# Performance work log

Hardware: AMD Instinct MI355X
Metric: run time of the kernel (lower is better)

## Reference

```python
import jax, jax.numpy as jnp
import numpy as np

KSIZE = 8
STRIDE = 4
HEADS = 8
DIM_HEAD = 32
EPS = 1e-5


def _layernorm(x, g, b):
    m = jnp.mean(x, axis=-1, keepdims=True)
    v = jnp.mean(jnp.square(x - m), axis=-1, keepdims=True)
    return (x - m) / jnp.sqrt(v + EPS) * g + b


def setup_inputs() -> dict:
    key = jax.random.key(0)
    ks = jax.random.split(key, 4)
    B, H, W, C = 8, 64, 64, 256
    inner = HEADS * DIM_HEAD  # 256
    x = jax.random.normal(ks[0], (B, H, W, C), dtype=jnp.float32)
    return {
        "x": x,
        "ln1_g": jnp.ones((C,), jnp.float32),
        "ln1_b": jnp.zeros((C,), jnp.float32),
        "ln2_g": jnp.ones((C,), jnp.float32),
        "ln2_b": jnp.zeros((C,), jnp.float32),
        "w_qkv": jax.random.normal(ks[1], (C, inner * 3), jnp.float32) * 0.02,
        "w_out": jax.random.normal(ks[2], (inner, C), jnp.float32) * 0.02,
        "b_out": jnp.zeros((C,), jnp.float32),
    }


def reference(x, ln1_g, ln1_b, ln2_g, ln2_b, w_qkv, w_out, b_out):
    B, H, W, C = x.shape
    k, s = KSIZE, STRIDE
    nH = (H - k) // s + 1
    nW = (W - k) // s + 1
    L = nH * nW
    n = k * k  # tokens per window

    # window index grids (im2col / unfold)
    rows = jnp.arange(nH)[:, None] * s + jnp.arange(k)[None, :]  # [nH, k]
    cols = jnp.arange(nW)[:, None] * s + jnp.arange(k)[None, :]  # [nW, k]
    ridx = rows[:, None, :, None]  # [nH,1,k,1]
    cidx = cols[None, :, None, :]  # [1,nW,1,k]

    # unfold: [B, nH, nW, k, k, C] -> [(B L), (k k), C]
    patches = x[:, ridx, cidx, :].reshape(B * L, n, C)

    # LocalAttention2D.norm then AttentionBlock.norm
    p = _layernorm(patches, ln1_g, ln1_b)
    h = _layernorm(p, ln2_g, ln2_b)

    qkv = h @ w_qkv  # [(B L), n, 3*inner]
    q, kk, v = jnp.split(qkv, 3, axis=-1)
    q = q.reshape(B * L, n, HEADS, DIM_HEAD)
    kk = kk.reshape(B * L, n, HEADS, DIM_HEAD)
    v = v.reshape(B * L, n, HEADS, DIM_HEAD)

    scale = DIM_HEAD ** -0.5
    dots = jnp.einsum('bnhd,bmhd->bhnm', q, kk) * scale
    attn = jax.nn.softmax(dots, axis=-1)
    o = jnp.einsum('bhnm,bmhd->bnhd', attn, v).reshape(B * L, n, HEADS * DIM_HEAD)
    o = o @ w_out + b_out  # [(B L), n, C]

    # fold (col2im overlap-add)
    o = o.reshape(B, nH, nW, k, k, C)
    out = jnp.zeros((B, H, W, C), x.dtype).at[:, ridx, cidx, :].add(o)

    # normalization: fold(unfold(ones)) == overlap counts
    counts = jnp.zeros((H, W), x.dtype).at[ridx, cidx].add(1.0)
    return out / counts[None, :, :, None]
```

## Files before the change

### kernel.cpp

```cpp
#include <hip/hip_runtime.h>
#include <hip/hip_bf16.h>
#include <cstdint>
#include <cstddef>

#define LN_EPS 1e-5f
#define B_    8
#define HW_   64
#define C_    256
#define NTOK  (B_ * HW_ * HW_)
#define HEADS_ 8
#define DH_    32

__global__ __launch_bounds__(256) void ln_stats_kernel(
    const float* __restrict__ x, const float* __restrict__ g1,
    const float* __restrict__ b1, float4* __restrict__ stats)
{
    const int gid  = blockIdx.x * 256 + threadIdx.x;
    const int tok  = gid >> 6;
    const int lane = gid & 63;
    if (tok >= NTOK) return;
    const float4 xv = reinterpret_cast<const float4*>(x + (size_t)tok * C_)[lane];
    float s  = xv.x + xv.y + xv.z + xv.w;
    float sq = xv.x*xv.x + xv.y*xv.y + xv.z*xv.z + xv.w*xv.w;
    for (int off = 32; off; off >>= 1) {
        s  += __shfl_xor(s, off);
        sq += __shfl_xor(sq, off);
    }
    const float m1 = s * (1.0f / 256.0f);
    const float r1 = rsqrtf(fmaxf(sq * (1.0f / 256.0f) - m1 * m1, 0.0f) + LN_EPS);
    const float4 g = reinterpret_cast<const float4*>(g1)[lane];
    const float4 b = reinterpret_cast<const float4*>(b1)[lane];
    const float y0 = (xv.x - m1) * r1 * g.x + b.x;
    const float y1 = (xv.y - m1) * r1 * g.y + b.y;
    const float y2 = (xv.z - m1) * r1 * g.z + b.z;
    const float y3 = (xv.w - m1) * r1 * g.w + b.w;
    float s2  = y0 + y1 + y2 + y3;
    float sq2 = y0*y0 + y1*y1 + y2*y2 + y3*y3;
    for (int off = 32; off; off >>= 1) {
        s2  += __shfl_xor(s2, off);
        sq2 += __shfl_xor(sq2, off);
    }
    const float m2 = s2 * (1.0f / 256.0f);
    const float r2 = rsqrtf(fmaxf(sq2 * (1.0f / 256.0f) - m2 * m2, 0.0f) + LN_EPS);
    if (lane == 0) stats[tok] = make_float4(m1, r1, m2, r2);
}

__global__ __launch_bounds__(256) void qkv_kernel(
    const float* __restrict__ x, const float4* __restrict__ stats,
    const float* __restrict__ g1, const float* __restrict__ b1,
    const float* __restrict__ g2, const float* __restrict__ b2,
    const float* __restrict__ w, float* __restrict__ qkv)
{
    __shared__ float At[16][72];
    __shared__ float Bt[16][64];
    const int tid  = threadIdx.x;
    const int tok0 = blockIdx.y * 64;
    const int n0   = blockIdx.x * 64;
    const int ty = tid >> 4, tx = tid & 15;
    const int st = tid >> 2, sseg = tid & 3;
    const int bk = tid >> 4, bx = tid & 15;
    const float4 s4 = stats[tok0 + st];
    const float* xrow = x + (size_t)(tok0 + st) * C_;
    float acc[4][4] = {};
    for (int kk = 0; kk < 16; ++kk) {
        const int k0 = kk * 16;
        const int ka = k0 + sseg * 4;
        const float4 xv  = *reinterpret_cast<const float4*>(xrow + ka);
        const float4 g1v = *reinterpret_cast<const float4*>(g1 + ka);
        const float4 b1v = *reinterpret_cast<const float4*>(b1 + ka);
        const float4 g2v = *reinterpret_cast<const float4*>(g2 + ka);
        const float4 b2v = *reinterpret_cast<const float4*>(b2 + ka);
        const float h0 = ((xv.x - s4.x)*s4.y*g1v.x + b1v.x - s4.z)*s4.w*g2v.x + b2v.x;
        const float h1 = ((xv.y - s4.x)*s4.y*g1v.y + b1v.y - s4.z)*s4.w*g2v.y + b2v.y;
        const float h2 = ((xv.z - s4.x)*s4.y*g1v.z + b1v.z - s4.z)*s4.w*g2v.z + b2v.z;
        const float h3 = ((xv.w - s4.x)*s4.y*g1v.w + b1v.w - s4.z)*s4.w*g2v.w + b2v.w;
        const float4 wv = *reinterpret_cast<const float4*>(w + (size_t)(k0 + bk) * 768 + n0 + bx * 4);
        __syncthreads();
        At[sseg*4+0][st] = h0;
        At[sseg*4+1][st] = h1;
        At[sseg*4+2][st] = h2;
        At[sseg*4+3][st] = h3;
        *reinterpret_cast<float4*>(&Bt[bk][bx*4]) = wv;
        __syncthreads();
        #pragma unroll
        for (int k = 0; k < 16; ++k) {
            const float4 a = *reinterpret_cast<const float4*>(&At[k][ty*4]);
            const float4 b = *reinterpret_cast<const float4*>(&Bt[k][tx*4]);
            acc[0][0] += a.x*b.x; acc[0][1] += a.x*b.y; acc[0][2] += a.x*b.z; acc[0][3] += a.x*b.w;
            acc[1][0] += a.y*b.x; acc[1][1] += a.y*b.y; acc[1][2] += a.y*b.z; acc[1][3] += a.y*b.w;
            acc[2][0] += a.z*b.x; acc[2][1] += a.z*b.y; acc[2][2] += a.z*b.z; acc[2][3] += a.z*b.w;
            acc[3][0] += a.w*b.x; acc[3][1] += a.w*b.y; acc[3][2] += a.w*b.z; acc[3][3] += a.w*b.w;
        }
    }
    #pragma unroll
    for (int r = 0; r < 4; ++r) {
        const float4 o = make_float4(acc[r][0], acc[r][1], acc[r][2], acc[r][3]);
        *reinterpret_cast<float4*>(qkv + (size_t)(tok0 + ty*4 + r) * 768 + n0 + tx*4) = o;
    }
}

__global__ __launch_bounds__(256) void attn_kernel(
    const float* __restrict__ qkv, float* __restrict__ out,
    int gi, int gj, int nJ)
{
    __shared__ float q_lds[64][36];
    __shared__ float k_lds[64][36];
    __shared__ float v_lds[64][36];
    __shared__ float p_lds[64][68];
    const int tid = threadIdx.x;
    const int b  = blockIdx.y;
    const int hd = blockIdx.z;
    const int pi = 2 * (blockIdx.x / nJ) + gi;
    const int pj = 2 * (blockIdx.x % nJ) + gj;
    const int t = tid >> 2, seg = tid & 3;
    const int pr = t >> 3, pc = t & 7;
    const size_t pixbase = ((size_t)((b * 64 + 4*pi + pr) * 64) + (4*pj + pc));
    {
        const size_t base = pixbase * 768 + hd * 32 + seg * 8;
        const float4 qa = *reinterpret_cast<const float4*>(qkv + base);
        const float4 qb = *reinterpret_cast<const float4*>(qkv + base + 4);
        const float4 ka = *reinterpret_cast<const float4*>(qkv + base + 256);
        const float4 kb = *reinterpret_cast<const float4*>(qkv + base + 260);
        const float4 va = *reinterpret_cast<const float4*>(qkv + base + 512);
        const float4 vb = *reinterpret_cast<const float4*>(qkv + base + 516);
        *reinterpret_cast<float4*>(&q_lds[t][seg*8    ]) = qa;
        *reinterpret_cast<float4*>(&q_lds[t][seg*8 + 4]) = qb;
        *reinterpret_cast<float4*>(&k_lds[t][seg*8    ]) = ka;
        *reinterpret_cast<float4*>(&k_lds[t][seg*8 + 4]) = kb;
        *reinterpret_cast<float4*>(&v_lds[t][seg*8    ]) = va;
        *reinterpret_cast<float4*>(&v_lds[t][seg*8 + 4]) = vb;
    }
    __syncthreads();
    const float scale = 0.17677669529663687f;
    float4 q4[8];
    #pragma unroll
    for (int u = 0; u < 8; ++u) q4[u] = *reinterpret_cast<const float4*>(&q_lds[t][u*4]);
    float p[16];
    #pragma unroll
    for (int jj = 0; jj < 16; ++jj) {
        const int jc = seg + jj * 4;
        float a0 = 0.f, a1 = 0.f, a2 = 0.f, a3 = 0.f;
        #pragma unroll
        for (int u = 0; u < 8; ++u) {
            const float4 kv = *reinterpret_cast<const float4*>(&k_lds[jc][u*4]);
            a0 = fmaf(q4[u].x, kv.x, a0);
            a1 = fmaf(q4[u].y, kv.y, a1);
            a2 = fmaf(q4[u].z, kv.z, a2);
            a3 = fmaf(q4[u].w, kv.w, a3);
        }
        p[jj] = ((a0 + a1) + (a2 + a3)) * scale;
    }
    float m = p[0];
    #pragma unroll
    for (int jj = 1; jj < 16; ++jj) m = fmaxf(m, p[jj]);
    m = fmaxf(m, __shfl_xor(m, 1));
    m = fmaxf(m, __shfl_xor(m, 2));
    float s = 0.f;
    #pragma unroll
    for (int jj = 0; jj < 16; ++jj) { p[jj] = __expf(p[jj] - m); s += p[jj]; }
    s += __shfl_xor(s, 1);
    s += __shfl_xor(s, 2);
    const float rs = 1.0f / s;
    #pragma unroll
    for (int jj = 0; jj < 16; ++jj) p_lds[t][seg + jj*4] = p[jj] * rs;
    __syncthreads();
    float4 o0 = make_float4(0,0,0,0), o1 = make_float4(0,0,0,0);
    for (int jc = 0; jc < 64; ++jc) {
        const float a = p_lds[t][jc];
        const float4 v0 = *reinterpret_cast<const float4*>(&v_lds[jc][seg*8]);
        const float4 v1 = *reinterpret_cast<const float4*>(&v_lds[jc][seg*8 + 4]);
        o0.x = fmaf(a, v0.x, o0.x); o0.y = fmaf(a, v0.y, o0.y);
        o0.z = fmaf(a, v0.z, o0.z); o0.w = fmaf(a, v0.w, o0.w);
        o1.x = fmaf(a, v1.x, o1.x); o1.y = fmaf(a, v1.y, o1.y);
        o1.z = fmaf(a, v1.z, o1.z); o1.w = fmaf(a, v1.w, o1.w);
    }
    float* op = out + pixbase * 256 + hd * 32 + seg * 8;
    float4 c0 = *reinterpret_cast<const float4*>(op);
    float4 c1 = *reinterpret_cast<const float4*>(op + 4);
    c0.x += o0.x; c0.y += o0.y; c0.z += o0.z; c0.w += o0.w;
    c1.x += o1.x; c1.y += o1.y; c1.z += o1.z; c1.w += o1.w;
    *reinterpret_cast<float4*>(op)     = c0;
    *reinterpret_cast<float4*>(op + 4) = c1;
}

__global__ __launch_bounds__(256) void proj_kernel(
    float* __restrict__ out, const float* __restrict__ w, const float* __restrict__ bo)
{
    __shared__ float At[16][36];
    __shared__ float Bt[16][256];
    const int tid  = threadIdx.x;
    const int tok0 = blockIdx.x * 32;
    const int ty = tid >> 5, tx = tid & 31;
    const int st = tid >> 2, sseg = tid & 3;
    const int bc = (tid & 63) * 4, bkb = tid >> 6;
    float ascale = 0.f;
    if (tid < 128) {
        const int token = tok0 + st;
        const int hp = (token >> 6) & 63, wp = token & 63;
        const float cnt = ((hp >= 4 && hp < 60) ? 2.f : 1.f) * ((wp >= 4 && wp < 60) ? 2.f : 1.f);
        ascale = 1.0f / cnt;
    }
    float acc[4][8] = {};
    for (int kk = 0; kk < 16; ++kk) {
        const int k0 = kk * 16;
        float4 av = make_float4(0,0,0,0);
        if (tid < 128)
            av = *reinterpret_cast<const float4*>(out + (size_t)(tok0 + st) * 256 + k0 + sseg * 4);
        float4 wv[4];
        #pragma unroll
        for (int u = 0; u < 4; ++u)
            wv[u] = *reinterpret_cast<const float4*>(w + (size_t)(k0 + bkb*4 + u) * 256 + bc);
        __syncthreads();
        if (tid < 128) {
            At[sseg*4+0][st] = av.x * ascale;
            At[sseg*4+1][st] = av.y * ascale;
            At[sseg*4+2][st] = av.z * ascale;
            At[sseg*4+3][st] = av.w * ascale;
        }
        #pragma unroll
        for (int u = 0; u < 4; ++u)
            *reinterpret_cast<float4*>(&Bt[bkb*4+u][bc]) = wv[u];
        __syncthreads();
        #pragma unroll
        for (int k = 0; k < 16; ++k) {
            const float4 a  = *reinterpret_cast<const float4*>(&At[k][ty*4]);
            const float4 b0 = *reinterpret_cast<const float4*>(&Bt[k][tx*4]);
            const float4 b1 = *reinterpret_cast<const float4*>(&Bt[k][128 + tx*4]);
            acc[0][0] += a.x*b0.x; acc[0][1] += a.x*b0.y; acc[0][2] += a.x*b0.z; acc[0][3] += a.x*b0.w;
            acc[0][4] += a.x*b1.x; acc[0][5] += a.x*b1.y; acc[0][6] += a.x*b1.z; acc[0][7] += a.x*b1.w;
            acc[1][0] += a.y*b0.x; acc[1][1] += a.y*b0.y; acc[1][2] += a.y*b0.z; acc[1][3] += a.y*b0.w;
            acc[1][4] += a.y*b1.x; acc[1][5] += a.y*b1.y; acc[1][6] += a.y*b1.z; acc[1][7] += a.y*b1.w;
            acc[2][0] += a.z*b0.x; acc[2][1] += a.z*b0.y; acc[2][2] += a.z*b0.z; acc[2][3] += a.z*b0.w;
            acc[2][4] += a.z*b1.x; acc[2][5] += a.z*b1.y; acc[2][6] += a.z*b1.z; acc[2][7] += a.z*b1.w;
            acc[3][0] += a.w*b0.x; acc[3][1] += a.w*b0.y; acc[3][2] += a.w*b0.z; acc[3][3] += a.w*b0.w;
            acc[3][4] += a.w*b1.x; acc[3][5] += a.w*b1.y; acc[3][6] += a.w*b1.z; acc[3][7] += a.w*b1.w;
        }
    }
    const float4 bo0 = *reinterpret_cast<const float4*>(bo + tx*4);
    const float4 bo1 = *reinterpret_cast<const float4*>(bo + 128 + tx*4);
    #pragma unroll
    for (int r = 0; r < 4; ++r) {
        float* orow = out + (size_t)(tok0 + ty*4 + r) * 256;
        const float4 o0 = make_float4(acc[r][0]+bo0.x, acc[r][1]+bo0.y, acc[r][2]+bo0.z, acc[r][3]+bo0.w);
        const float4 o1 = make_float4(acc[r][4]+bo1.x, acc[r][5]+bo1.y, acc[r][6]+bo1.z, acc[r][7]+bo1.w);
        *reinterpret_cast<float4*>(orow + tx*4)       = o0;
        *reinterpret_cast<float4*>(orow + 128 + tx*4) = o1;
    }
}

extern "C" void kernel_launch(void* const* d_in, const int* in_sizes, int n_in,
                              void* d_out, int out_size, void* d_ws, size_t ws_size,
                              hipStream_t stream)
{
    const float* x     = (const float*)d_in[0];
    const float* ln1_g = (const float*)d_in[1];
    const float* ln1_b = (const float*)d_in[2];
    const float* ln2_g = (const float*)d_in[3];
    const float* ln2_b = (const float*)d_in[4];
    const float* w_qkv = (const float*)d_in[5];
    const float* w_out = (const float*)d_in[6];
    const float* b_out = (const float*)d_in[7];
    float* out = (float*)d_out;
    float* ws  = (float*)d_ws;

    float4* stats = (float4*)ws;
    float*  qkv   = ws + (size_t)NTOK * 4;

    ln_stats_kernel<<<NTOK / 4, 256, 0, stream>>>(x, ln1_g, ln1_b, stats);
    qkv_kernel<<<dim3(12, NTOK / 64), 256, 0, stream>>>(x, stats, ln1_g, ln1_b, ln2_g, ln2_b, w_qkv, qkv);
    hipMemsetAsync(d_out, 0, (size_t)out_size * sizeof(float), stream);
    for (int g = 0; g < 4; ++g) {
        const int gi = g >> 1, gj = g & 1;
        const int nI = gi ? 7 : 8, nJ = gj ? 7 : 8;
        attn_kernel<<<dim3(nI * nJ, B_, HEADS_), 256, 0, stream>>>(qkv, out, gi, gj, nJ);
    }
    proj_kernel<<<NTOK / 32, 256, 0, stream>>>(out, w_out, b_out);
}
```

Before: 473.8 us.

## Enlarge QKV GEMM tile to 128x128 with 8x8 per-thread register blocking

Replaces the 64x64x16 tile with 4x4 outputs per thread by a 128x128x32 tile with 8x8 outputs per thread in the fused layernorm+QKV projection. Each thread now loads and normalizes more activation and weight data per stage, and the launch grid shrinks to match. The goal is higher arithmetic intensity per LDS and global load and fewer block-level syncs. The cost is higher register pressure from 64 accumulators, which may lower occupancy, plus more LDS per block.

```diff
diff --git a/kernel.cpp b/kernel.cpp
--- a/kernel.cpp
+++ b/kernel.cpp
@@ -51,51 +51,83 @@
     const float* __restrict__ g2, const float* __restrict__ b2,
     const float* __restrict__ w, float* __restrict__ qkv)
 {
-    __shared__ float At[16][72];
-    __shared__ float Bt[16][64];
+    __shared__ float At[32][130];
+    __shared__ float Bt[32][132];
     const int tid  = threadIdx.x;
-    const int tok0 = blockIdx.y * 64;
-    const int n0   = blockIdx.x * 64;
+    const int tok0 = blockIdx.y * 128;
+    const int n0   = blockIdx.x * 128;
     const int ty = tid >> 4, tx = tid & 15;
-    const int st = tid >> 2, sseg = tid & 3;
-    const int bk = tid >> 4, bx = tid & 15;
-    const float4 s4 = stats[tok0 + st];
-    const float* xrow = x + (size_t)(tok0 + st) * C_;
-    float acc[4][4] = {};
-    for (int kk = 0; kk < 16; ++kk) {
-        const int k0 = kk * 16;
-        const int ka = k0 + sseg * 4;
-        const float4 xv  = *reinterpret_cast<const float4*>(xrow + ka);
-        const float4 g1v = *reinterpret_cast<const float4*>(g1 + ka);
-        const float4 b1v = *reinterpret_cast<const float4*>(b1 + ka);
-        const float4 g2v = *reinterpret_cast<const float4*>(g2 + ka);
-        const float4 b2v = *reinterpret_cast<const float4*>(b2 + ka);
-        const float h0 = ((xv.x - s4.x)*s4.y*g1v.x + b1v.x - s4.z)*s4.w*g2v.x + b2v.x;
-        const float h1 = ((xv.y - s4.x)*s4.y*g1v.y + b1v.y - s4.z)*s4.w*g2v.y + b2v.y;
-        const float h2 = ((xv.z - s4.x)*s4.y*g1v.z + b1v.z - s4.z)*s4.w*g2v.z + b2v.z;
-        const float h3 = ((xv.w - s4.x)*s4.y*g1v.w + b1v.w - s4.z)*s4.w*g2v.w + b2v.w;
-        const float4 wv = *reinterpret_cast<const float4*>(w + (size_t)(k0 + bk) * 768 + n0 + bx * 4);
+    const int ar  = tid >> 1;
+    const int asb = (tid & 1) * 4;
+
+    const float4 s4 = stats[tok0 + ar];
+    const float m1 = s4.x, r1 = s4.y, m2 = s4.z, r2 = s4.w;
+    const float* xrow = x + (size_t)(tok0 + ar) * C_;
+
+    float acc[8][8] = {};
+
+    for (int it = 0; it < 8; ++it) {
+        const int k0 = it * 32;
+        float4 av[4];
+        #pragma unroll
+        for (int u = 0; u < 4; ++u) {
+            const int ka = k0 + (asb + u) * 4;
+            const float4 xv  = *reinterpret_cast<const float4*>(xrow + ka);
+            const float4 g1v = *reinterpret_cast<const float4*>(g1 + ka);
+            const float4 b1v = *reinterpret_cast<const float4*>(b1 + ka);
+            const float4 g2v = *reinterpret_cast<const float4*>(g2 + ka);
+            const float4 b2v = *reinterpret_cast<const float4*>(b2 + ka);
+            av[u].x = ((xv.x - m1) * r1 * g1v.x + b1v.x - m2) * r2 * g2v.x + b2v.x;
+            av[u].y = ((xv.y - m1) * r1 * g1v.y + b1v.y - m2) * r2 * g2v.y + b2v.y;
+            av[u].z = ((xv.z - m1) * r1 * g1v.z + b1v.z - m2) * r2 * g2v.z + b2v.z;
+            av[u].w = ((xv.w - m1) * r1 * g1v.w + b1v.w - m2) * r2 * g2v.w + b2v.w;
+        }
+        float4 bv[4];
+        #pragma unroll
+        for (int rep = 0; rep < 4; ++rep) {
+            const int e  = rep * 256 + tid;
+            const int bk = e >> 5, bc = (e & 31) * 4;
+            bv[rep] = *reinterpret_cast<const float4*>(w + (size_t)(k0 + bk) * 768 + n0 + bc);
+        }
         __syncthreads();
-        At[sseg*4+0][st] = h0;
-        At[sseg*4+1][st] = h1;
-        At[sseg*4+2][st] = h2;
-        At[sseg*4+3][st] = h3;
-        *reinterpret_cast<float4*>(&Bt[bk][bx*4]) = wv;
+        #pragma unroll
+        for (int u = 0; u < 4; ++u) {
+            const int kk = (asb + u) * 4;
+            At[kk + 0][ar] = av[u].x;
+            At[kk + 1][ar] = av[u].y;
+            At[kk + 2][ar] = av[u].z;
+            At[kk + 3][ar] = av[u].w;
+        }
+        #pragma unroll
+        for (int rep = 0; rep < 4; ++rep) {
+            const int e  = rep * 256 + tid;
+            const int bk = e >> 5, bc = (e & 31) * 4;
+            *reinterpret_cast<float4*>(&Bt[bk][bc]) = bv[rep];
+        }
         __syncthreads();
         #pragma unroll
-        for (int k = 0; k < 16; ++k) {
-            const float4 a = *reinterpret_cast<const float4*>(&At[k][ty*4]);
-            const float4 b = *reinterpret_cast<const float4*>(&Bt[k][tx*4]);
-            acc[0][0] += a.x*b.x; acc[0][1] += a.x*b.y; acc[0][2] += a.x*b.z; acc[0][3] += a.x*b.w;
-            acc[1][0] += a.y*b.x; acc[1][1] += a.y*b.y; acc[1][2] += a.y*b.z; acc[1][3] += a.y*b.w;
-            acc[2][0] += a.z*b.x; acc[2][1] += a.z*b.y; acc[2][2] += a.z*b.z; acc[2][3] += a.z*b.w;
-            acc[3][0] += a.w*b.x; acc[3][1] += a.w*b.y; acc[3][2] += a.w*b.z; acc[3][3] += a.w*b.w;
-        }
-    }
-    #pragma unroll
-    for (int r = 0; r < 4; ++r) {
-        const float4 o = make_float4(acc[r][0], acc[r][1], acc[r][2], acc[r][3]);
-        *reinterpret_cast<float4*>(qkv + (size_t)(tok0 + ty*4 + r) * 768 + n0 + tx*4) = o;
+        for (int k = 0; k < 32; ++k) {
+            const float4 a0 = *reinterpret_cast<const float4*>(&At[k][ty*8]);
+            const float4 a1 = *reinterpret_cast<const float4*>(&At[k][ty*8 + 4]);
+            const float4 b0 = *reinterpret_cast<const float4*>(&Bt[k][tx*4]);
+            const float4 b1 = *reinterpret_cast<const float4*>(&Bt[k][64 + tx*4]);
+            const float a[8] = {a0.x, a0.y, a0.z, a0.w, a1.x, a1.y, a1.z, a1.w};
+            const float b[8] = {b0.x, b0.y, b0.z, b0.w, b1.x, b1.y, b1.z, b1.w};
+            #pragma unroll
+            for (int i = 0; i < 8; ++i) {
+                #pragma unroll
+                for (int j = 0; j < 8; ++j)
+                    acc[i][j] = fmaf(a[i], b[j], acc[i][j]);
+            }
+        }
+    }
+    #pragma unroll
+    for (int i = 0; i < 8; ++i) {
+        float* orow = qkv + (size_t)(tok0 + ty*8 + i) * 768 + n0;
+        *reinterpret_cast<float4*>(orow + tx*4) =
+            make_float4(acc[i][0], acc[i][1], acc[i][2], acc[i][3]);
+        *reinterpret_cast<float4*>(orow + 64 + tx*4) =
+            make_float4(acc[i][4], acc[i][5], acc[i][6], acc[i][7]);
     }
 }
 
@@ -267,7 +299,8 @@
     float*  qkv   = ws + (size_t)NTOK * 4;
 
     ln_stats_kernel<<<NTOK / 4, 256, 0, stream>>>(x, ln1_g, ln1_b, stats);
-    qkv_kernel<<<dim3(12, NTOK / 64), 256, 0, stream>>>(x, stats, ln1_g, ln1_b, ln2_g, ln2_b, w_qkv, qkv);
+    qkv_kernel<<<dim3(6, NTOK / 128), 256, 0, stream>>>(
+        x, stats, ln1_g, ln1_b, ln2_g, ln2_b, w_qkv, qkv);
     hipMemsetAsync(d_out, 0, (size_t)out_size * sizeof(float), stream);
     for (int g = 0; g < 4; ++g) {
         const int gi = g >> 1, gj = g & 1;
```

Measured after the change: 465.2 us. Within noise of the previous version (-1.8%).

## Register-tile QK^T with transposed K and drop output memset

Applied to the files above, without the earlier changes.

The QK^T stage in the attention kernel now gives each thread a 4x4 tile of scores, reading K from a transposed shared-memory layout. This cuts shared-memory reads per FMA compared with each thread computing 16 separate dot products. The softmax row reductions now go through 16-lane shuffles. The hipMemsetAsync on the output is removed: the first window-parity group writes its results directly, since its windows tile the image without overlap, and the later groups accumulate as before. The scattered transposed K stores may cause some shared-memory bank conflicts.

```diff
diff --git a/kernel.cpp b/kernel.cpp
--- a/kernel.cpp
+++ b/kernel.cpp
@@ -101,10 +101,10 @@
 
 __global__ __launch_bounds__(256) void attn_kernel(
     const float* __restrict__ qkv, float* __restrict__ out,
-    int gi, int gj, int nJ)
+    int gi, int gj, int nJ, int do_store)
 {
     __shared__ float q_lds[64][36];
-    __shared__ float k_lds[64][36];
+    __shared__ float kT[32][68];
     __shared__ float v_lds[64][36];
     __shared__ float p_lds[64][68];
     const int tid = threadIdx.x;
@@ -125,44 +125,70 @@
         const float4 vb = *reinterpret_cast<const float4*>(qkv + base + 516);
         *reinterpret_cast<float4*>(&q_lds[t][seg*8    ]) = qa;
         *reinterpret_cast<float4*>(&q_lds[t][seg*8 + 4]) = qb;
-        *reinterpret_cast<float4*>(&k_lds[t][seg*8    ]) = ka;
-        *reinterpret_cast<float4*>(&k_lds[t][seg*8 + 4]) = kb;
         *reinterpret_cast<float4*>(&v_lds[t][seg*8    ]) = va;
         *reinterpret_cast<float4*>(&v_lds[t][seg*8 + 4]) = vb;
+        const int d0 = seg * 8;
+        kT[d0+0][t] = ka.x; kT[d0+1][t] = ka.y; kT[d0+2][t] = ka.z; kT[d0+3][t] = ka.w;
+        kT[d0+4][t] = kb.x; kT[d0+5][t] = kb.y; kT[d0+6][t] = kb.z; kT[d0+7][t] = kb.w;
     }
     __syncthreads();
     const float scale = 0.17677669529663687f;
-    float4 q4[8];
-    #pragma unroll
-    for (int u = 0; u < 8; ++u) q4[u] = *reinterpret_cast<const float4*>(&q_lds[t][u*4]);
-    float p[16];
-    #pragma unroll
-    for (int jj = 0; jj < 16; ++jj) {
-        const int jc = seg + jj * 4;
-        float a0 = 0.f, a1 = 0.f, a2 = 0.f, a3 = 0.f;
-        #pragma unroll
-        for (int u = 0; u < 8; ++u) {
-            const float4 kv = *reinterpret_cast<const float4*>(&k_lds[jc][u*4]);
-            a0 = fmaf(q4[u].x, kv.x, a0);
-            a1 = fmaf(q4[u].y, kv.y, a1);
-            a2 = fmaf(q4[u].z, kv.z, a2);
-            a3 = fmaf(q4[u].w, kv.w, a3);
-        }
-        p[jj] = ((a0 + a1) + (a2 + a3)) * scale;
-    }
-    float m = p[0];
-    #pragma unroll
-    for (int jj = 1; jj < 16; ++jj) m = fmaxf(m, p[jj]);
-    m = fmaxf(m, __shfl_xor(m, 1));
-    m = fmaxf(m, __shfl_xor(m, 2));
-    float s = 0.f;
-    #pragma unroll
-    for (int jj = 0; jj < 16; ++jj) { p[jj] = __expf(p[jj] - m); s += p[jj]; }
-    s += __shfl_xor(s, 1);
-    s += __shfl_xor(s, 2);
-    const float rs = 1.0f / s;
-    #pragma unroll
-    for (int jj = 0; jj < 16; ++jj) p_lds[t][seg + jj*4] = p[jj] * rs;
+    const int tr = tid >> 4, tc = tid & 15;
+    float s[4][4] = {};
+    #pragma unroll
+    for (int kk = 0; kk < 4; ++kk) {
+        float qreg[4][8];
+        #pragma unroll
+        for (int i = 0; i < 4; ++i) {
+            const float4 qv0 = *reinterpret_cast<const float4*>(&q_lds[tr*4 + i][kk*8]);
+            const float4 qv1 = *reinterpret_cast<const float4*>(&q_lds[tr*4 + i][kk*8 + 4]);
+            qreg[i][0] = qv0.x; qreg[i][1] = qv0.y; qreg[i][2] = qv0.z; qreg[i][3] = qv0.w;
+            qreg[i][4] = qv1.x; qreg[i][5] = qv1.y; qreg[i][6] = qv1.z; qreg[i][7] = qv1.w;
+        }
+        #pragma unroll
+        for (int w = 0; w < 8; ++w) {
+            const float4 kv = *reinterpret_cast<const float4*>(&kT[kk*8 + w][tc*4]);
+            const float ka[4] = {kv.x, kv.y, kv.z, kv.w};
+            #pragma unroll
+            for (int i = 0; i < 4; ++i) {
+                #pragma unroll
+                for (int j = 0; j < 4; ++j)
+                    s[i][j] = fmaf(qreg[i][w], ka[j], s[i][j]);
+            }
+        }
+    }
+    float mrow[4], sum[4];
+    #pragma unroll
+    for (int i = 0; i < 4; ++i) {
+        s[i][0] *= scale; s[i][1] *= scale; s[i][2] *= scale; s[i][3] *= scale;
+        mrow[i] = fmaxf(fmaxf(s[i][0], s[i][1]), fmaxf(s[i][2], s[i][3]));
+    }
+    #pragma unroll
+    for (int off = 1; off < 16; off <<= 1)
+        #pragma unroll
+        for (int i = 0; i < 4; ++i)
+            mrow[i] = fmaxf(mrow[i], __shfl_xor(mrow[i], off));
+    #pragma unroll
+    for (int i = 0; i < 4; ++i) {
+        sum[i] = 0.f;
+        #pragma unroll
+        for (int j = 0; j < 4; ++j) {
+            s[i][j] = __expf(s[i][j] - mrow[i]);
+            sum[i] += s[i][j];
+        }
+    }
+    #pragma unroll
+    for (int off = 1; off < 16; off <<= 1)
+        #pragma unroll
+        for (int i = 0; i < 4; ++i)
+            sum[i] += __shfl_xor(sum[i], off);
+    #pragma unroll
+    for (int i = 0; i < 4; ++i) {
+        const float rs = 1.0f / sum[i];
+        #pragma unroll
+        for (int j = 0; j < 4; ++j)
+            p_lds[tr*4 + i][tc*4 + j] = s[i][j] * rs;
+    }
     __syncthreads();
     float4 o0 = make_float4(0,0,0,0), o1 = make_float4(0,0,0,0);
     for (int jc = 0; jc < 64; ++jc) {
@@ -175,12 +201,17 @@
         o1.z = fmaf(a, v1.z, o1.z); o1.w = fmaf(a, v1.w, o1.w);
     }
     float* op = out + pixbase * 256 + hd * 32 + seg * 8;
-    float4 c0 = *reinterpret_cast<const float4*>(op);
-    float4 c1 = *reinterpret_cast<const float4*>(op + 4);
-    c0.x += o0.x; c0.y += o0.y; c0.z += o0.z; c0.w += o0.w;
-    c1.x += o1.x; c1.y += o1.y; c1.z += o1.z; c1.w += o1.w;
-    *reinterpret_cast<float4*>(op)     = c0;
-    *reinterpret_cast<float4*>(op + 4) = c1;
+    if (do_store) {
+        *reinterpret_cast<float4*>(op)     = o0;
+        *reinterpret_cast<float4*>(op + 4) = o1;
+    } else {
+        float4 c0 = *reinterpret_cast<const float4*>(op);
+        float4 c1 = *reinterpret_cast<const float4*>(op + 4);
+        c0.x += o0.x; c0.y += o0.y; c0.z += o0.z; c0.w += o0.w;
+        c1.x += o1.x; c1.y += o1.y; c1.z += o1.z; c1.w += o1.w;
+        *reinterpret_cast<float4*>(op)     = c0;
+        *reinterpret_cast<float4*>(op + 4) = c1;
+    }
 }
 
 __global__ __launch_bounds__(256) void proj_kernel(
@@ -267,12 +298,13 @@
     float*  qkv   = ws + (size_t)NTOK * 4;
 
     ln_stats_kernel<<<NTOK / 4, 256, 0, stream>>>(x, ln1_g, ln1_b, stats);
-    qkv_kernel<<<dim3(12, NTOK / 64), 256, 0, stream>>>(x, stats, ln1_g, ln1_b, ln2_g, ln2_b, w_qkv, qkv);
-    hipMemsetAsync(d_out, 0, (size_t)out_size * sizeof(float), stream);
+    qkv_kernel<<<dim3(12, NTOK / 64), 256, 0, stream>>>(
+        x, stats, ln1_g, ln1_b, ln2_g, ln2_b, w_qkv, qkv);
     for (int g = 0; g < 4; ++g) {
         const int gi = g >> 1, gj = g & 1;
         const int nI = gi ? 7 : 8, nJ = gj ? 7 : 8;
-        attn_kernel<<<dim3(nI * nJ, B_, HEADS_), 256, 0, stream>>>(qkv, out, gi, gj, nJ);
+        attn_kernel<<<dim3(nI * nJ, B_, HEADS_), 256, 0, stream>>>(
+            qkv, out, gi, gj, nJ, (g == 0) ? 1 : 0);
     }
     proj_kernel<<<NTOK / 32, 256, 0, stream>>>(out, w_out, b_out);
 }
```

Measured after the change: 459.6 us. -3.0%, faster.
